# Kernel tuning notes

Hardware: AMD Instinct MI355X
Metric: run time of the kernel (lower is better)

## Reference

```python
import jax, jax.numpy as jnp
import numpy as np

MAXDISP = 192


def setup_inputs() -> dict:
    key = jax.random.key(0)
    x = jax.random.normal(key, (2, 1, 48, 64, 128), dtype=jnp.float32)
    return {"x": x}


def reference(x):
    B, C, D, H, W = x.shape  # C == 1, low-res cost volume
    # Trilinear upsample, align_corners=False (half-pixel centers) ==
    # jax.image.resize method='linear'. Target: [B,1,maxdisp+1, 4H, 4W].
    vol = jax.image.resize(x, (B, C, MAXDISP + 1, H * 4, W * 4), method="linear")
    vol = vol[:, 0]  # squeeze channel -> [B, D', H', W']
    # Softmin over disparity = softmax(-vol, axis=1)
    probs = jax.nn.softmax(-vol, axis=1)
    disp = jnp.arange(MAXDISP + 1, dtype=probs.dtype)
    out = jnp.einsum("bdhw,d->bhw", probs, disp)  # [B, 4H, 4W]
    return out
```

## Files before the change

### kernel.cpp

```cpp
#include <hip/hip_runtime.h>

#define D_IN  48
#define H_IN  64
#define W_IN  128
#define D_OUT 193
#define H_OUT 256
#define W_OUT 512
#define NCOL  34

typedef float f32x2 __attribute__((ext_vector_type(2)));


__device__ __forceinline__ float exp2_fast(float x) {
#if __has_builtin(__builtin_amdgcn_exp2f)
    return __builtin_amdgcn_exp2f(x);
#else
    float r;
    asm("v_exp_f32 %0, %1" : "=v"(r) : "v"(x));
    return r;
#endif
}

template<int Q>
__device__ __forceinline__ void compute_quarter2(const float* base, f32x2 fw2,
                                                 f32x2& s_out, f32x2& ds_out) {
    constexpr int K0   = (Q == 0) ? 0  : (Q == 1) ? 11 : (Q == 2) ? 23  : 35;
    constexpr int KHI  = (Q == 0) ? 11 : (Q == 1) ? 23 : (Q == 2) ? 35  : 46;
    constexpr int DMIN = (Q == 0) ? 2  : (Q == 1) ? 49 : (Q == 2) ? 97  : 145;
    constexpr int DMAX = (Q == 0) ? 48 : (Q == 1) ? 96 : (Q == 2) ? 144 : 190;

    const float* pr = base + K0 * NCOL;
    float a0 = pr[0], b0 = pr[1];
    f32x2 g = __builtin_elementwise_fma(fw2, (f32x2){b0 - a0, b0 - a0},
                                        (f32x2){a0, a0});

    f32x2 s = {0.f, 0.f}, ds = {0.f, 0.f};

    if (Q == 0) {
        f32x2 e = { exp2_fast(g.x), exp2_fast(g.y) };
        s = e + e;
        ds = e;
    }

    #pragma unroll
    for (int k = K0; k <= KHI; ++k) {
        const float* pn = base + (k + 1) * NCOL;
        float an = pn[0], bn = pn[1];
        f32x2 gn = __builtin_elementwise_fma(fw2, (f32x2){bn - an, bn - an},
                                             (f32x2){an, an});
        f32x2 delta = gn - g;
        int dlo = (386 * k + 240) / 96;           if (dlo < DMIN) dlo = DMIN;
        int dhi = (386 * (k + 1) + 240) / 96 - 1; if (dhi > DMAX) dhi = DMAX;

        float f0 = (float)(96 * dlo - 145 - 386 * k) * (1.0f / 386.0f);
        f32x2 arg0 = __builtin_elementwise_fma((f32x2){f0, f0}, delta, g);
        f32x2 e = { exp2_fast(arg0.x), exp2_fast(arg0.y) };
        f32x2 rarg = delta * (96.0f / 386.0f);
        f32x2 r = { exp2_fast(rarg.x), exp2_fast(rarg.y) };

        #pragma unroll
        for (int d = dlo; d <= dhi; ++d) {
            s = s + e;
            f32x2 dv = {(float)d, (float)d};
            ds = __builtin_elementwise_fma(dv, e, ds);
            if (d != dhi) e = e * r;
        }
        g = gn;
    }

    if (Q == 3) {
        f32x2 e = { exp2_fast(g.x), exp2_fast(g.y) };
        s = s + e + e;
        ds = __builtin_elementwise_fma((f32x2){383.f, 383.f}, e, ds);
    }

    s_out = s;
    ds_out = ds;
}

__global__ __launch_bounds__(256) void disp_kernel(const float* __restrict__ x,
                                                   float* __restrict__ out) {
    __shared__ float sm[D_IN * NCOL];
    __shared__ f32x2 red_s[256], red_d[256];

    int t = threadIdx.x;
    int slot = t & 63;
    int qq = t >> 6;
    int p0 = blockIdx.x << 7;
    int pA = p0 + 2 * slot;
    int wA = pA & (W_OUT - 1);
    int h = (pA >> 9) & (H_OUT - 1);
    int b = pA >> 17;
    int wblk = p0 & (W_OUT - 1);

    float hf = (h + 0.5f) * 0.25f - 0.5f;
    float hfl = floorf(hf);
    int h0 = (int)hfl;
    float fh = hf - hfl;
    int hp; float fhp;
    if (h0 < 0)              { hp = 0;        fhp = 0.f; }
    else if (h0 >= H_IN - 1) { hp = H_IN - 2; fhp = 1.f; }
    else                     { hp = h0;       fhp = fh;  }

    int wp; float fA, fB;
    if (wA == 0)              { wp = 0;              fA = 0.f;    fB = 0.f;    }
    else if (wA == W_OUT - 2) { wp = W_IN - 2;       fA = 1.f;    fB = 1.f;    }
    else if (wA & 2)          { wp = wA >> 2;        fA = 0.125f; fB = 0.375f; }
    else                      { wp = (wA >> 2) - 1;  fA = 0.625f; fB = 0.875f; }
    f32x2 fw2 = {fA, fB};

    const float L2E = 1.4426950408889634f;
    int col0 = (wblk >> 2) - 1; if (col0 < 0) col0 = 0;
    const float* xrow = x + (size_t)b * (D_IN * H_IN * W_IN) + hp * W_IN;
    float fhn = -L2E * fhp;
    {
        int j = t % NCOL;
        int k = t / NCOL;
        for (int idx = t; idx < D_IN * NCOL; idx += 256) {
            int col = col0 + j; if (col > W_IN - 1) col = W_IN - 1;
            const float* q = xrow + k * (H_IN * W_IN) + col;
            float a = q[0], bq = q[W_IN];
            sm[idx] = fmaf(fhn, bq - a, a * (-L2E));
            j += 256 - 7 * NCOL;
            k += 7;
            if (j >= NCOL) { j -= NCOL; k += 1; }
        }
    }
    __syncthreads();

    const float* base = &sm[wp - col0];
    f32x2 S, D;
    if      (qq == 0) compute_quarter2<0>(base, fw2, S, D);
    else if (qq == 1) compute_quarter2<1>(base, fw2, S, D);
    else if (qq == 2) compute_quarter2<2>(base, fw2, S, D);
    else              compute_quarter2<3>(base, fw2, S, D);

    red_s[t] = S; red_d[t] = D;
    __syncthreads();

    if (t < 64) {
        f32x2 den = (red_s[t] + red_s[t + 64]) + (red_s[t + 128] + red_s[t + 192]);
        f32x2 num = (red_d[t] + red_d[t + 64]) + (red_d[t + 128] + red_d[t + 192]);
        int p = p0 + 2 * t;
#if __has_builtin(__builtin_amdgcn_rcpf)
        out[p]     = num.x * __builtin_amdgcn_rcpf(den.x);
        out[p + 1] = num.y * __builtin_amdgcn_rcpf(den.y);
#else
        out[p]     = num.x / den.x;
        out[p + 1] = num.y / den.y;
#endif
    }
}

extern "C" void kernel_launch(void* const* d_in, const int* in_sizes, int n_in,
                              void* d_out, int out_size, void* d_ws, size_t ws_size,
                              hipStream_t stream) {
    const float* x = (const float*)d_in[0];
    float* out = (float*)d_out;
    int total_pixels = 2 * H_OUT * W_OUT;
    int blocks = total_pixels / 128;
    disp_kernel<<<blocks, 256, 0, stream>>>(x, out);
}
```

Measured before the change: 13.38 us.

## Process four output pixels per thread with vectorized shared-memory staging

Each block now covers 256 output pixels instead of 128, and each thread computes two pixel pairs that share one low-res input column. The shared-memory tile widens to 72 columns and is filled with aligned float4 loads, and outputs go out as a float4 store. This halves the block count and amortizes the H-interpolation staging and reduction per pixel, at the cost of more registers per thread and a larger LDS footprint.

```diff
diff --git a/kernel.cpp b/kernel.cpp
--- a/kernel.cpp
+++ b/kernel.cpp
@@ -6,9 +6,10 @@
 #define D_OUT 193
 #define H_OUT 256
 #define W_OUT 512
-#define NCOL  34
+#define NCOL  72
 
 typedef float f32x2 __attribute__((ext_vector_type(2)));
+typedef float f32x4 __attribute__((ext_vector_type(4)));
 
 
 __device__ __forceinline__ float exp2_fast(float x) {
@@ -22,75 +23,93 @@
 }
 
 template<int Q>
-__device__ __forceinline__ void compute_quarter2(const float* base, f32x2 fw2,
-                                                 f32x2& s_out, f32x2& ds_out) {
+__device__ __forceinline__ void compute_quarter4(const float* base1, const float* base2,
+                                                 f32x2 f1, f32x2 f2,
+                                                 f32x2& s1o, f32x2& ds1o,
+                                                 f32x2& s2o, f32x2& ds2o) {
     constexpr int K0   = (Q == 0) ? 0  : (Q == 1) ? 11 : (Q == 2) ? 23  : 35;
     constexpr int KHI  = (Q == 0) ? 11 : (Q == 1) ? 23 : (Q == 2) ? 35  : 46;
     constexpr int DMIN = (Q == 0) ? 2  : (Q == 1) ? 49 : (Q == 2) ? 97  : 145;
     constexpr int DMAX = (Q == 0) ? 48 : (Q == 1) ? 96 : (Q == 2) ? 144 : 190;
 
-    const float* pr = base + K0 * NCOL;
-    float a0 = pr[0], b0 = pr[1];
-    f32x2 g = __builtin_elementwise_fma(fw2, (f32x2){b0 - a0, b0 - a0},
-                                        (f32x2){a0, a0});
+    const float* p1 = base1 + K0 * NCOL;
+    const float* p2 = base2 + K0 * NCOL;
+    float a1 = p1[0], b1 = p1[1], a2 = p2[0], b2 = p2[1];
+    float d1 = b1 - a1, d2 = b2 - a2;
+    f32x2 g1 = __builtin_elementwise_fma(f1, (f32x2){d1, d1}, (f32x2){a1, a1});
+    f32x2 g2 = __builtin_elementwise_fma(f2, (f32x2){d2, d2}, (f32x2){a2, a2});
 
-    f32x2 s = {0.f, 0.f}, ds = {0.f, 0.f};
+    f32x2 s1 = {0.f,0.f}, ds1 = {0.f,0.f}, s2 = {0.f,0.f}, ds2 = {0.f,0.f};
 
     if (Q == 0) {
-        f32x2 e = { exp2_fast(g.x), exp2_fast(g.y) };
-        s = e + e;
-        ds = e;
+        f32x2 e1 = { exp2_fast(g1.x), exp2_fast(g1.y) };
+        f32x2 e2 = { exp2_fast(g2.x), exp2_fast(g2.y) };
+        s1 = e1 + e1;  ds1 = e1;
+        s2 = e2 + e2;  ds2 = e2;
     }
 
     #pragma unroll
     for (int k = K0; k <= KHI; ++k) {
-        const float* pn = base + (k + 1) * NCOL;
-        float an = pn[0], bn = pn[1];
-        f32x2 gn = __builtin_elementwise_fma(fw2, (f32x2){bn - an, bn - an},
-                                             (f32x2){an, an});
-        f32x2 delta = gn - g;
+        const float* q1 = base1 + (k + 1) * NCOL;
+        const float* q2 = base2 + (k + 1) * NCOL;
+        float na1 = q1[0], nb1 = q1[1], na2 = q2[0], nb2 = q2[1];
+        float nd1 = nb1 - na1, nd2 = nb2 - na2;
+        f32x2 gn1 = __builtin_elementwise_fma(f1, (f32x2){nd1, nd1}, (f32x2){na1, na1});
+        f32x2 gn2 = __builtin_elementwise_fma(f2, (f32x2){nd2, nd2}, (f32x2){na2, na2});
+        f32x2 del1 = gn1 - g1;
+        f32x2 del2 = gn2 - g2;
+
         int dlo = (386 * k + 240) / 96;           if (dlo < DMIN) dlo = DMIN;
         int dhi = (386 * (k + 1) + 240) / 96 - 1; if (dhi > DMAX) dhi = DMAX;
 
         float f0 = (float)(96 * dlo - 145 - 386 * k) * (1.0f / 386.0f);
-        f32x2 arg0 = __builtin_elementwise_fma((f32x2){f0, f0}, delta, g);
-        f32x2 e = { exp2_fast(arg0.x), exp2_fast(arg0.y) };
-        f32x2 rarg = delta * (96.0f / 386.0f);
-        f32x2 r = { exp2_fast(rarg.x), exp2_fast(rarg.y) };
+        f32x2 e1, e2, r1, r2;
+        {
+            f32x2 arg1 = __builtin_elementwise_fma((f32x2){f0, f0}, del1, g1);
+            f32x2 arg2 = __builtin_elementwise_fma((f32x2){f0, f0}, del2, g2);
+            e1 = (f32x2){ exp2_fast(arg1.x), exp2_fast(arg1.y) };
+            e2 = (f32x2){ exp2_fast(arg2.x), exp2_fast(arg2.y) };
+            f32x2 ra1 = del1 * (96.0f / 386.0f);
+            f32x2 ra2 = del2 * (96.0f / 386.0f);
+            r1 = (f32x2){ exp2_fast(ra1.x), exp2_fast(ra1.y) };
+            r2 = (f32x2){ exp2_fast(ra2.x), exp2_fast(ra2.y) };
+        }
 
         #pragma unroll
         for (int d = dlo; d <= dhi; ++d) {
-            s = s + e;
             f32x2 dv = {(float)d, (float)d};
-            ds = __builtin_elementwise_fma(dv, e, ds);
-            if (d != dhi) e = e * r;
+            s1 = s1 + e1;
+            ds1 = __builtin_elementwise_fma(dv, e1, ds1);
+            s2 = s2 + e2;
+            ds2 = __builtin_elementwise_fma(dv, e2, ds2);
+            if (d != dhi) { e1 = e1 * r1; e2 = e2 * r2; }
         }
-        g = gn;
+        g1 = gn1; g2 = gn2;
     }
 
     if (Q == 3) {
-        f32x2 e = { exp2_fast(g.x), exp2_fast(g.y) };
-        s = s + e + e;
-        ds = __builtin_elementwise_fma((f32x2){383.f, 383.f}, e, ds);
+        f32x2 e1 = { exp2_fast(g1.x), exp2_fast(g1.y) };
+        f32x2 e2 = { exp2_fast(g2.x), exp2_fast(g2.y) };
+        f32x2 c383 = {383.f, 383.f};
+        s1 = s1 + e1 + e1;  ds1 = __builtin_elementwise_fma(c383, e1, ds1);
+        s2 = s2 + e2 + e2;  ds2 = __builtin_elementwise_fma(c383, e2, ds2);
     }
 
-    s_out = s;
-    ds_out = ds;
+    s1o = s1; ds1o = ds1; s2o = s2; ds2o = ds2;
 }
 
 __global__ __launch_bounds__(256) void disp_kernel(const float* __restrict__ x,
                                                    float* __restrict__ out) {
     __shared__ float sm[D_IN * NCOL];
-    __shared__ f32x2 red_s[256], red_d[256];
+    __shared__ f32x2 red_s1[256], red_d1[256], red_s2[256], red_d2[256];
 
     int t = threadIdx.x;
     int slot = t & 63;
     int qq = t >> 6;
-    int p0 = blockIdx.x << 7;
-    int pA = p0 + 2 * slot;
-    int wA = pA & (W_OUT - 1);
-    int h = (pA >> 9) & (H_OUT - 1);
-    int b = pA >> 17;
+    int p0 = blockIdx.x << 8;
+    int pix = p0 + 4 * slot;
+    int h = (pix >> 9) & (H_OUT - 1);
+    int b = pix >> 17;
     int wblk = p0 & (W_OUT - 1);
 
     float hf = (h + 0.5f) * 0.25f - 0.5f;
@@ -102,53 +121,67 @@
     else if (h0 >= H_IN - 1) { hp = H_IN - 2; fhp = 1.f; }
     else                     { hp = h0;       fhp = fh;  }
 
-    int wp; float fA, fB;
-    if (wA == 0)              { wp = 0;              fA = 0.f;    fB = 0.f;    }
-    else if (wA == W_OUT - 2) { wp = W_IN - 2;       fA = 1.f;    fB = 1.f;    }
-    else if (wA & 2)          { wp = wA >> 2;        fA = 0.125f; fB = 0.375f; }
-    else                      { wp = (wA >> 2) - 1;  fA = 0.625f; fB = 0.875f; }
-    f32x2 fw2 = {fA, fB};
+    int u0 = wblk >> 2;
+    int u = u0 + slot;
+    int wp1; f32x2 f1;
+    if (u == 0) { wp1 = 0;     f1 = (f32x2){0.f, 0.f}; }
+    else        { wp1 = u - 1; f1 = (f32x2){0.625f, 0.875f}; }
+    int wp2; f32x2 f2;
+    if (u == 127) { wp2 = 126; f2 = (f32x2){1.f, 1.f}; }
+    else          { wp2 = u;   f2 = (f32x2){0.125f, 0.375f}; }
 
     const float L2E = 1.4426950408889634f;
-    int col0 = (wblk >> 2) - 1; if (col0 < 0) col0 = 0;
+    int col0 = u0 - 1; if (col0 < 0) col0 = 0;
+    int col0a = col0 & ~3;
     const float* xrow = x + (size_t)b * (D_IN * H_IN * W_IN) + hp * W_IN;
     float fhn = -L2E * fhp;
-    {
-        int j = t % NCOL;
-        int k = t / NCOL;
-        for (int idx = t; idx < D_IN * NCOL; idx += 256) {
-            int col = col0 + j; if (col > W_IN - 1) col = W_IN - 1;
-            const float* q = xrow + k * (H_IN * W_IN) + col;
-            float a = q[0], bq = q[W_IN];
-            sm[idx] = fmaf(fhn, bq - a, a * (-L2E));
-            j += 256 - 7 * NCOL;
-            k += 7;
-            if (j >= NCOL) { j -= NCOL; k += 1; }
+    for (int idx = t; idx < D_IN * (NCOL / 4); idx += 256) {
+        int k  = idx / (NCOL / 4);
+        int jc = idx - k * (NCOL / 4);
+        int col = col0a + 4 * jc;
+        const float* q = xrow + k * (H_IN * W_IN) + col;
+        f32x4 a, bq;
+        if (col <= W_IN - 4) {
+            a  = *(const f32x4*)(q);
+            bq = *(const f32x4*)(q + W_IN);
+        } else {
+            const float* qe = xrow + k * (H_IN * W_IN) + (W_IN - 1);
+            float av = qe[0], bv = qe[W_IN];
+            a  = (f32x4){av, av, av, av};
+            bq = (f32x4){bv, bv, bv, bv};
         }
+        f32x4 v = (bq - a) * fhn + a * (-L2E);
+        *(f32x4*)(&sm[k * NCOL + 4 * jc]) = v;
     }
     __syncthreads();
 
-    const float* base = &sm[wp - col0];
-    f32x2 S, D;
-    if      (qq == 0) compute_quarter2<0>(base, fw2, S, D);
-    else if (qq == 1) compute_quarter2<1>(base, fw2, S, D);
-    else if (qq == 2) compute_quarter2<2>(base, fw2, S, D);
-    else              compute_quarter2<3>(base, fw2, S, D);
+    const float* base1 = &sm[wp1 - col0a];
+    const float* base2 = &sm[wp2 - col0a];
+    f32x2 S1, D1, S2, D2;
+    if      (qq == 0) compute_quarter4<0>(base1, base2, f1, f2, S1, D1, S2, D2);
+    else if (qq == 1) compute_quarter4<1>(base1, base2, f1, f2, S1, D1, S2, D2);
+    else if (qq == 2) compute_quarter4<2>(base1, base2, f1, f2, S1, D1, S2, D2);
+    else              compute_quarter4<3>(base1, base2, f1, f2, S1, D1, S2, D2);
 
-    red_s[t] = S; red_d[t] = D;
+    red_s1[t] = S1; red_d1[t] = D1; red_s2[t] = S2; red_d2[t] = D2;
     __syncthreads();
 
     if (t < 64) {
-        f32x2 den = (red_s[t] + red_s[t + 64]) + (red_s[t + 128] + red_s[t + 192]);
-        f32x2 num = (red_d[t] + red_d[t + 64]) + (red_d[t + 128] + red_d[t + 192]);
-        int p = p0 + 2 * t;
+        f32x2 den1 = (red_s1[t] + red_s1[t + 64]) + (red_s1[t + 128] + red_s1[t + 192]);
+        f32x2 num1 = (red_d1[t] + red_d1[t + 64]) + (red_d1[t + 128] + red_d1[t + 192]);
+        f32x2 den2 = (red_s2[t] + red_s2[t + 64]) + (red_s2[t + 128] + red_s2[t + 192]);
+        f32x2 num2 = (red_d2[t] + red_d2[t + 64]) + (red_d2[t + 128] + red_d2[t + 192]);
+        f32x4 o;
 #if __has_builtin(__builtin_amdgcn_rcpf)
-        out[p]     = num.x * __builtin_amdgcn_rcpf(den.x);
-        out[p + 1] = num.y * __builtin_amdgcn_rcpf(den.y);
+        o.x = num1.x * __builtin_amdgcn_rcpf(den1.x);
+        o.y = num1.y * __builtin_amdgcn_rcpf(den1.y);
+        o.z = num2.x * __builtin_amdgcn_rcpf(den2.x);
+        o.w = num2.y * __builtin_amdgcn_rcpf(den2.y);
 #else
-        out[p]     = num.x / den.x;
-        out[p + 1] = num.y / den.y;
+        o.x = num1.x / den1.x;  o.y = num1.y / den1.y;
+        o.z = num2.x / den2.x;  o.w = num2.y / den2.y;
 #endif
+        *(f32x4*)(&out[p0 + 4 * t]) = o;
     }
 }
 
@@ -158,6 +191,6 @@
     const float* x = (const float*)d_in[0];
     float* out = (float*)d_out;
     int total_pixels = 2 * H_OUT * W_OUT;
-    int blocks = total_pixels / 128;
+    int blocks = total_pixels / 256;
     disp_kernel<<<blocks, 256, 0, stream>>>(x, out);
 }
```

New measurement: 13.02 us. -2.7%, faster.
